# Optimization experiments

Measured on AMD Instinct MI355X. Metric: run time of the kernel, lower is better.

Reference implementation:

```python
import jax, jax.numpy as jnp
import numpy as np

SIGMA = 1.0
BN_EPS = 1e-5
N_OP, N_MACH, N_JOB = 200000, 1000, 20000
E_OM, E_JO, N_PAIRS = 1000000, 200000, 500000
H, D0 = 64, 32


def _bn(x, g, b):
    # BatchNorm1d, training-mode batch statistics over the node/row dim
    m = x.mean(0)
    v = x.var(0)
    return g * (x - m) * jax.lax.rsqrt(v + BN_EPS) + b


def _encode(x, W):
    # MultiPeriodicEncoder: learned frequencies, concat(sin, cos) -> 2*16 = 32 dims
    h = (x @ W) / SIGMA
    return jnp.concatenate([jnp.sin(h), jnp.cos(h)], axis=-1)


def _gin(x_dst, agg, eps, W1, b1, g1, be1, W2, b2):
    # GINConv: MLP((1+eps)*x + sum-aggregated messages); MLP = Lin->BN->ReLU->Lin
    h = ((1.0 + eps) * x_dst + agg) @ W1 + b1
    h = jax.nn.relu(_bn(h, g1, be1))
    return h @ W2 + b2


def _forward(x_operation, x_machine, x_job,
             W_enc_op, W_enc_mach, W_enc_job,
             gin_W1_l0, gin_W1_l12, gin_b1, gin_g1, gin_be1, gin_W2, gin_b2, gin_eps,
             Ws1, bs1, gs1, bes1, Ws2, bs2, gs2, bes2, Ws3, bs3,
             e_om_src, e_om_dst, e_mo_src, e_mo_dst, e_jo_src, e_jo_dst,
             e_oj_src, e_oj_dst, vp_op, vp_mach, vp_job):
    x_op = _encode(x_operation, W_enc_op)    # [N_OP, 32]
    x_ma = _encode(x_machine, W_enc_mach)    # [N_MACH, 32]
    x_jb = _encode(x_job, W_enc_job)         # [N_JOB, 32]
    num_layers = gin_eps.shape[0]
    for l in range(num_layers):
        def p(e):
            W1 = gin_W1_l0[e] if l == 0 else gin_W1_l12[l - 1, e]
            return (gin_eps[l, e], W1, gin_b1[l, e], gin_g1[l, e],
                    gin_be1[l, e], gin_W2[l, e], gin_b2[l, e])
        # edge-type order: 0=op->mach, 1=mach->op, 2=job->op, 3=op->job
        agg_mach = jax.ops.segment_sum(x_op[e_om_src], e_om_dst, num_segments=N_MACH)
        agg_op_mo = jax.ops.segment_sum(x_ma[e_mo_src], e_mo_dst, num_segments=N_OP)
        agg_op_jo = jax.ops.segment_sum(x_jb[e_jo_src], e_jo_dst, num_segments=N_OP)
        agg_job = jax.ops.segment_sum(x_op[e_oj_src], e_oj_dst, num_segments=N_JOB)
        new_ma = _gin(x_ma, agg_mach, *p(0))
        new_op = _gin(x_op, agg_op_mo, *p(1)) + _gin(x_op, agg_op_jo, *p(2))  # hetero 'sum'
        new_jb = _gin(x_jb, agg_job, *p(3))
        if l > 0:  # residual add of previous layer output (= current input)
            new_op = new_op + x_op
            new_ma = new_ma + x_ma
            new_jb = new_jb + x_jb
        x_op, x_ma, x_jb = new_op, new_ma, new_jb
    # gather by valid_pairs, concat in node-type order [operation, machine, job]
    feat = jnp.concatenate([x_op[vp_op], x_ma[vp_mach], x_jb[vp_job]], axis=1)  # [P, 192]
    h = jax.nn.relu(_bn(feat @ Ws1 + bs1, gs1, bes1))
    h = jax.nn.relu(_bn(h @ Ws2 + bs2, gs2, bes2))
    return (h @ Ws3 + bs3)[:, 0]


def setup_inputs() -> dict:
    key = jax.random.key(0)
    ks = jax.random.split(key, 24)
    rn = lambda k, s: jax.random.normal(k, s, dtype=jnp.float32) * 0.1
    return {
        'x_operation': jax.random.normal(ks[0], (N_OP, 8), dtype=jnp.float32),
        'x_machine': jax.random.normal(ks[1], (N_MACH, 4), dtype=jnp.float32),
        'x_job': jax.random.normal(ks[2], (N_JOB, 4), dtype=jnp.float32),
        'W_enc_op': rn(ks[3], (8, 16)),
        'W_enc_mach': rn(ks[4], (4, 16)),
        'W_enc_job': rn(ks[5], (4, 16)),
        'gin_W1_l0': rn(ks[6], (4, D0, H)),
        'gin_W1_l12': rn(ks[7], (2, 4, H, H)),
        'gin_b1': jnp.zeros((3, 4, H), jnp.float32),
        'gin_g1': jnp.ones((3, 4, H), jnp.float32),
        'gin_be1': jnp.zeros((3, 4, H), jnp.float32),
        'gin_W2': rn(ks[8], (3, 4, H, H)),
        'gin_b2': jnp.zeros((3, 4, H), jnp.float32),
        'gin_eps': jnp.zeros((3, 4), jnp.float32),
        'Ws1': rn(ks[9], (3 * H, H)),
        'bs1': jnp.zeros((H,), jnp.float32),
        'gs1': jnp.ones((H,), jnp.float32),
        'bes1': jnp.zeros((H,), jnp.float32),
        'Ws2': rn(ks[10], (H, H // 2)),
        'bs2': jnp.zeros((H // 2,), jnp.float32),
        'gs2': jnp.ones((H // 2,), jnp.float32),
        'bes2': jnp.zeros((H // 2,), jnp.float32),
        'Ws3': rn(ks[11], (H // 2, 1)),
        'bs3': jnp.zeros((1,), jnp.float32),
        'e_om_src': jax.random.randint(ks[12], (E_OM,), 0, N_OP),
        'e_om_dst': jax.random.randint(ks[13], (E_OM,), 0, N_MACH),
        'e_mo_src': jax.random.randint(ks[14], (E_OM,), 0, N_MACH),
        'e_mo_dst': jax.random.randint(ks[15], (E_OM,), 0, N_OP),
        'e_jo_src': jax.random.randint(ks[16], (E_JO,), 0, N_JOB),
        'e_jo_dst': jax.random.randint(ks[17], (E_JO,), 0, N_OP),
        'e_oj_src': jax.random.randint(ks[18], (E_JO,), 0, N_OP),
        'e_oj_dst': jax.random.randint(ks[19], (E_JO,), 0, N_JOB),
        'vp_op': jax.random.randint(ks[20], (N_PAIRS,), 0, N_OP),
        'vp_mach': jax.random.randint(ks[21], (N_PAIRS,), 0, N_MACH),
        'vp_job': jax.random.randint(ks[22], (N_PAIRS,), 0, N_JOB),
    }


def reference(x_operation, x_machine, x_job,
              W_enc_op, W_enc_mach, W_enc_job,
              gin_W1_l0, gin_W1_l12, gin_b1, gin_g1, gin_be1, gin_W2, gin_b2, gin_eps,
              Ws1, bs1, gs1, bes1, Ws2, bs2, gs2, bes2, Ws3, bs3,
              e_om_src, e_om_dst, e_mo_src, e_mo_dst, e_jo_src, e_jo_dst,
              e_oj_src, e_oj_dst, vp_op, vp_mach, vp_job):
    return _forward(x_operation, x_machine, x_job,
                    W_enc_op, W_enc_mach, W_enc_job,
                    gin_W1_l0, gin_W1_l12, gin_b1, gin_g1, gin_be1, gin_W2, gin_b2, gin_eps,
                    Ws1, bs1, gs1, bes1, Ws2, bs2, gs2, bes2, Ws3, bs3,
                    e_om_src, e_om_dst, e_mo_src, e_mo_dst, e_jo_src, e_jo_dst,
                    e_oj_src, e_oj_dst, vp_op, vp_mach, vp_job)
```

## Files before the change

kernel.cpp:

```cpp
#include <hip/hip_runtime.h>
#include <math.h>

#define N_OP_   200000
#define N_MACH_ 1000
#define N_JOB_  20000
#define E_OM_   1000000
#define E_JO_   200000
#define N_PAIRS_ 500000

#define B_OM_ 0
#define B_MO_ 64000
#define B_JO_ 264000
#define B_OJ_ 464000
#define TOTC_ 484000
#define E_TOT_ 2400000

#define GH_   1172
#define G_OP_ 782
#define G_MA_ 4
#define G_JB_ 79

#define CDIV(a,b) (((a)+(b)-1)/(b))

typedef __attribute__((ext_vector_type(8))) short short8v;
typedef __attribute__((ext_vector_type(4))) float f32x4;

__device__ __forceinline__ unsigned short f2bf(float f){
  unsigned int u = __float_as_uint(f);
  return (unsigned short)((u + 0x7fffu + ((u>>16)&1u)) >> 16);
}
__device__ __forceinline__ float bf2f(unsigned short h){
  return __uint_as_float(((unsigned int)h)<<16);
}

template<int DIN>
__device__ __forceinline__ void encode_body(const float* __restrict__ x,
    const float* __restrict__ W, float* __restrict__ out, int N, float* sW, int bid){
  if (threadIdx.x < DIN*16) sW[threadIdx.x] = W[threadIdx.x];
  __syncthreads();
  int i = bid*256 + threadIdx.x;
  if (i >= N) return;
  float xv[DIN];
#pragma unroll
  for (int k=0;k<DIN;k++) xv[k] = x[i*DIN+k];
#pragma unroll
  for (int j=0;j<16;j++){
    float h = 0.f;
#pragma unroll
    for (int k=0;k<DIN;k++) h = fmaf(xv[k], sW[k*16+j], h);
    float s, c;
    sincosf(h, &s, &c);
    out[(size_t)i*64 + j]      = s;
    out[(size_t)i*64 + 16 + j] = c;
  }
}

__device__ __forceinline__ int edge_cidx(int e,
    const int* __restrict__ eom_d, const int* __restrict__ emo_d,
    const int* __restrict__ ejo_d, const int* __restrict__ eoj_d){
  if (e < E_OM_)            return B_OM_ + eom_d[e]*64 + (e & 63);
  else if (e < 2*E_OM_)     return B_MO_ + emo_d[e - E_OM_];
  else if (e < 2*E_OM_+E_JO_) return B_JO_ + ejo_d[e - 2*E_OM_];
  else                      return B_OJ_ + eoj_d[e - 2*E_OM_ - E_JO_];
}
__device__ __forceinline__ int edge_src(int e,
    const int* __restrict__ eom_s, const int* __restrict__ emo_s,
    const int* __restrict__ ejo_s, const int* __restrict__ eoj_s){
  if (e < E_OM_)            return eom_s[e];
  else if (e < 2*E_OM_)     return emo_s[e - E_OM_];
  else if (e < 2*E_OM_+E_JO_) return ejo_s[e - 2*E_OM_];
  else                      return eoj_s[e - 2*E_OM_ - E_JO_];
}

__global__ __launch_bounds__(256) void enc_hist_kernel(
    const float* __restrict__ xop, const float* __restrict__ Wop, float* __restrict__ Pop,
    const float* __restrict__ xma, const float* __restrict__ Wma, float* __restrict__ Pma,
    const float* __restrict__ xjb, const float* __restrict__ Wjb, float* __restrict__ Pjb,
    const int* __restrict__ eom_d, const int* __restrict__ emo_d,
    const int* __restrict__ ejo_d, const int* __restrict__ eoj_d,
    int* __restrict__ cnt)
{
  __shared__ float sW[128];
  int b = blockIdx.x;
  if (b < GH_){
    const int gsz = GH_*256;
    int i0 = b*256 + threadIdx.x;
    for (int base = i0; base < E_TOT_; base += 8*gsz){
      int c[8]; bool act[8];
#pragma unroll
      for (int j=0;j<8;j++){
        int e = base + j*gsz;
        act[j] = (e < E_TOT_);
        if (act[j]) c[j] = edge_cidx(e, eom_d, emo_d, ejo_d, eoj_d);
      }
#pragma unroll
      for (int j=0;j<8;j++) if (act[j]) atomicAdd(&cnt[c[j]], 1);
    }
  } else if (b < GH_ + G_OP_){
    encode_body<8>(xop, Wop, Pop, N_OP_, sW, b - GH_);
  } else if (b < GH_ + G_OP_ + G_MA_){
    encode_body<4>(xma, Wma, Pma, N_MACH_, sW, b - GH_ - G_OP_);
  } else {
    encode_body<4>(xjb, Wjb, Pjb, N_JOB_, sW, b - GH_ - G_OP_ - G_MA_);
  }
}

__global__ __launch_bounds__(256) void fill_all_kernel(
    const int* __restrict__ eom_s, const int* __restrict__ eom_d,
    const int* __restrict__ emo_s, const int* __restrict__ emo_d,
    const int* __restrict__ ejo_s, const int* __restrict__ ejo_d,
    const int* __restrict__ eoj_s, const int* __restrict__ eoj_d,
    int* __restrict__ cursor, int* __restrict__ elist){
  int gsz = gridDim.x*blockDim.x;
  int i0 = blockIdx.x*blockDim.x + threadIdx.x;
  for (int base = i0; base < E_TOT_; base += 8*gsz){
    int cidx[8], src[8]; bool act[8];
#pragma unroll
    for (int j=0;j<8;j++){
      int e = base + j*gsz;
      act[j] = (e < E_TOT_);
      if (act[j]){
        cidx[j] = edge_cidx(e, eom_d, emo_d, ejo_d, eoj_d);
        src[j]  = edge_src (e, eom_s, emo_s, ejo_s, eoj_s);
      }
    }
    int p[8];
#pragma unroll
    for (int j=0;j<8;j++) if (act[j]) p[j] = atomicAdd(&cursor[cidx[j]], 1);
#pragma unroll
    for (int j=0;j<8;j++) if (act[j]) elist[p[j]] = src[j];
  }
}

__global__ void scan_block_sums(const int* __restrict__ cnt, int N, int* __restrict__ partials){
  __shared__ int red[256];
  int base = blockIdx.x*2048;
  int s = 0;
#pragma unroll
  for (int j=0;j<8;j++){ int i = base + threadIdx.x + j*256; if (i<N) s += cnt[i]; }
  red[threadIdx.x] = s; __syncthreads();
  for (int st=128; st>0; st>>=1){ if (threadIdx.x<st) red[threadIdx.x]+=red[threadIdx.x+st]; __syncthreads(); }
  if (threadIdx.x==0) partials[blockIdx.x] = red[0];
}

__global__ void scan_partials(int* __restrict__ partials, int NB, int* __restrict__ offN){
  __shared__ int buf[256];
  int v = (threadIdx.x < NB) ? partials[threadIdx.x] : 0;
  buf[threadIdx.x] = v; __syncthreads();
  int acc = v;
  for (int st=1; st<256; st<<=1){
    int t = (threadIdx.x >= st) ? buf[threadIdx.x-st] : 0;
    __syncthreads();
    acc += t; buf[threadIdx.x] = acc;
    __syncthreads();
  }
  if (threadIdx.x < NB) partials[threadIdx.x] = acc - v;
  if (threadIdx.x == NB-1) offN[0] = acc;
}

__global__ void scan_write_offsets(const int* __restrict__ cnt, int N,
    const int* __restrict__ partials, int* __restrict__ off){
  __shared__ int buf[256];
  int base = blockIdx.x*2048;
  int v[8]; int s = 0;
#pragma unroll
  for (int j=0;j<8;j++){ int i = base + threadIdx.x*8 + j; v[j] = (i<N)?cnt[i]:0; s += v[j]; }
  buf[threadIdx.x] = s; __syncthreads();
  int acc = s;
  for (int st=1; st<256; st<<=1){
    int t = (threadIdx.x >= st) ? buf[threadIdx.x-st] : 0;
    __syncthreads();
    acc += t; buf[threadIdx.x] = acc;
    __syncthreads();
  }
  int ex = partials[blockIdx.x] + acc - s;
#pragma unroll
  for (int j=0;j<8;j++){ int i = base + threadIdx.x*8 + j; if (i<N) off[i] = ex; ex += v[j]; }
}

__global__ __launch_bounds__(256) void agg_block_kernel(const int* __restrict__ off,
    const int* __restrict__ srcs, const float* __restrict__ feat,
    float* __restrict__ outp, int Ndst, int D){
  __shared__ float red[4][64];
  int m = blockIdx.x;
  if (m >= Ndst) return;
  int g = threadIdx.x >> 6, lane = threadIdx.x & 63;
  int s = off[m*64], e = off[m*64 + 64];
  float acc = 0.f;
  for (int base = s + g*64; base < e; base += 256){
    int cnt = e - base; if (cnt > 64) cnt = 64;
    int r = (lane < cnt) ? srcs[base + lane] : 0;
    int i = 0;
    for (; i + 4 <= cnt; i += 4){
      int r0 = __shfl(r, i), r1 = __shfl(r, i+1), r2 = __shfl(r, i+2), r3 = __shfl(r, i+3);
      float v0 = feat[(size_t)r0*64 + lane];
      float v1 = feat[(size_t)r1*64 + lane];
      float v2 = feat[(size_t)r2*64 + lane];
      float v3 = feat[(size_t)r3*64 + lane];
      acc += (v0 + v1) + (v2 + v3);
    }
    for (; i < cnt; i++){
      int ri = __shfl(r, i);
      acc += feat[(size_t)ri*64 + lane];
    }
  }
  red[g][lane] = acc;
  __syncthreads();
  if (g==0 && lane<D)
    outp[(size_t)m*64+lane] = red[0][lane]+red[1][lane]+red[2][lane]+red[3][lane];
}

template<int K>
__global__ __launch_bounds__(256,3) void partA_fused_kernel(
    const int* __restrict__ off_all, const int* __restrict__ elist,
    const float* __restrict__ Xop, const float* __restrict__ Xma, const float* __restrict__ Xjb,
    float* hm, float* ho1, float* ho2, float* hj,
    const float* __restrict__ Wm, const float* __restrict__ Wa,
    const float* __restrict__ Wb, const float* __restrict__ Wj,
    const float* __restrict__ bm, const float* __restrict__ ba,
    const float* __restrict__ bb, const float* __restrict__ bj,
    float* __restrict__ lstats,
    const float* __restrict__ epsp, int ebase)
{
  constexpr int KP = K + 4;
  constexpr int NF4 = K/16;
  __shared__ float sW[K][64];
  __shared__ float sZ[64][KP];
  __shared__ float sred[16][64];
  const int tid = threadIdx.x;
  const int lc = tid & 15, lr = tid >> 4;
  const int Tm = (N_MACH_+63)>>6, To = (N_OP_+63)>>6;
  int t = blockIdx.x;
  int seg, tile;
  if (t < Tm){ seg=0; tile=t; }
  else if (t < Tm+To){ seg=1; tile=t-Tm; }
  else if (t < Tm+2*To){ seg=2; tile=t-Tm-To; }
  else { seg=3; tile=t-Tm-2*To; }
  float* z            = seg==0?hm:seg==1?ho1:seg==2?ho2:hj;
  const float* x      = seg==0?Xma:seg==3?Xjb:Xop;
  const float* feat   = seg==0?Xop:seg==1?Xma:seg==2?Xjb:Xop;
  const float* W      = seg==0?Wm:seg==1?Wa:seg==2?Wb:Wj;
  const float* b      = seg==0?bm:seg==1?ba:seg==2?bb:bj;
  const int N         = seg==0?N_MACH_:seg==3?N_JOB_:N_OP_;
  const int* offs     = off_all + (seg==0?B_OM_:seg==1?B_MO_:seg==2?B_JO_:B_OJ_);
  float* st           = lstats + seg*128;
  const float e1 = 1.0f + epsp[ebase + seg];
  for (int idx = tid*4; idx < K*64; idx += 1024){
    int k = idx >> 6, c = idx & 63;
    *(float4*)&sW[k][c] = *(const float4*)&W[(size_t)k*64 + c];
  }
  float4 bias4 = *(const float4*)&b[lc*4];
  const int rbase = tile << 6;
  {
    const int r = tid >> 2, q = tid & 3;
    const int cbase = q*(K/4);
    int row = rbase + r;
    float4 a4[NF4];
#pragma unroll
    for (int f=0; f<NF4; f++) a4[f] = make_float4(0.f,0.f,0.f,0.f);
    if (row < N){
      if (seg == 0){
        const float4* H4 = (const float4*)&z[(size_t)row*64 + cbase];
#pragma unroll
        for (int f=0; f<NF4; f++) a4[f] = H4[f];
      } else {
        int s = offs[row], e = offs[row+1];
        int i = s;
        for (; i+2<=e; i+=2){
          int s0 = elist[i], s1 = elist[i+1];
          const float4* F0 = (const float4*)&feat[(size_t)s0*64 + cbase];
          const float4* F1 = (const float4*)&feat[(size_t)s1*64 + cbase];
          float4 v0[NF4], v1[NF4];
#pragma unroll
          for (int f=0; f<NF4; f++){ v0[f]=F0[f]; v1[f]=F1[f]; }
#pragma unroll
          for (int f=0; f<NF4; f++){
            a4[f].x += v0[f].x + v1[f].x;
            a4[f].y += v0[f].y + v1[f].y;
            a4[f].z += v0[f].z + v1[f].z;
            a4[f].w += v0[f].w + v1[f].w;
          }
        }
        if (i < e){
          int s0 = elist[i];
          const float4* F0 = (const float4*)&feat[(size_t)s0*64 + cbase];
#pragma unroll
          for (int f=0; f<NF4; f++){
            float4 v = F0[f];
            a4[f].x += v.x; a4[f].y += v.y; a4[f].z += v.z; a4[f].w += v.w;
          }
        }
      }
      const float4* X4 = (const float4*)&x[(size_t)row*64 + cbase];
#pragma unroll
      for (int f=0; f<NF4; f++){
        float4 xv = X4[f];
        a4[f].x = fmaf(e1, xv.x, a4[f].x);
        a4[f].y = fmaf(e1, xv.y, a4[f].y);
        a4[f].z = fmaf(e1, xv.z, a4[f].z);
        a4[f].w = fmaf(e1, xv.w, a4[f].w);
      }
    }
#pragma unroll
    for (int f=0; f<NF4; f++) *(float4*)&sZ[r][cbase + f*4] = a4[f];
  }
  __syncthreads();
  float acc[4][4];
#pragma unroll
  for (int i=0;i<4;i++){ acc[i][0]=0.f; acc[i][1]=0.f; acc[i][2]=0.f; acc[i][3]=0.f; }
#pragma unroll 2
  for (int kb = 0; kb < K/4; kb++){
    float4 zf[4], wf[4];
#pragma unroll
    for (int i=0;i<4;i++) zf[i] = *(const float4*)&sZ[lr*4+i][kb*4];
#pragma unroll
    for (int kk=0;kk<4;kk++) wf[kk] = *(const float4*)&sW[kb*4+kk][lc*4];
#pragma unroll
    for (int i=0;i<4;i++){
      acc[i][0] = fmaf(zf[i].x, wf[0].x, acc[i][0]);
      acc[i][1] = fmaf(zf[i].x, wf[0].y, acc[i][1]);
      acc[i][2] = fmaf(zf[i].x, wf[0].z, acc[i][2]);
      acc[i][3] = fmaf(zf[i].x, wf[0].w, acc[i][3]);
      acc[i][0] = fmaf(zf[i].y, wf[1].x, acc[i][0]);
      acc[i][1] = fmaf(zf[i].y, wf[1].y, acc[i][1]);
      acc[i][2] = fmaf(zf[i].y, wf[1].z, acc[i][2]);
      acc[i][3] = fmaf(zf[i].y, wf[1].w, acc[i][3]);
      acc[i][0] = fmaf(zf[i].z, wf[2].x, acc[i][0]);
      acc[i][1] = fmaf(zf[i].z, wf[2].y, acc[i][1]);
      acc[i][2] = fmaf(zf[i].z, wf[2].z, acc[i][2]);
      acc[i][3] = fmaf(zf[i].z, wf[2].w, acc[i][3]);
      acc[i][0] = fmaf(zf[i].w, wf[3].x, acc[i][0]);
      acc[i][1] = fmaf(zf[i].w, wf[3].y, acc[i][1]);
      acc[i][2] = fmaf(zf[i].w, wf[3].z, acc[i][2]);
      acc[i][3] = fmaf(zf[i].w, wf[3].w, acc[i][3]);
    }
  }
  float4 psum = make_float4(0.f,0.f,0.f,0.f), psq = make_float4(0.f,0.f,0.f,0.f);
#pragma unroll
  for (int i=0;i<4;i++){
    int row = rbase + lr*4 + i;
    if (row < N){
      float4 o;
      o.x = acc[i][0] + bias4.x;
      o.y = acc[i][1] + bias4.y;
      o.z = acc[i][2] + bias4.z;
      o.w = acc[i][3] + bias4.w;
      *(float4*)&z[(size_t)row*64 + lc*4] = o;
      psum.x += o.x; psum.y += o.y; psum.z += o.z; psum.w += o.w;
      psq.x += o.x*o.x; psq.y += o.y*o.y; psq.z += o.z*o.z; psq.w += o.w*o.w;
    }
  }
  __syncthreads();
  *(float4*)&sred[lr][lc*4] = psum;
  __syncthreads();
  if (tid < 64){
    float s = 0.f;
#pragma unroll
    for (int j=0;j<16;j++) s += sred[j][tid];
    atomicAdd(&st[tid], s);
  }
  __syncthreads();
  *(float4*)&sred[lr][lc*4] = psq;
  __syncthreads();
  if (tid < 64){
    float s = 0.f;
#pragma unroll
    for (int j=0;j<16;j++) s += sred[j][tid];
    atomicAdd(&st[64+tid], s);
  }
}

template<bool RESID>
__global__ __launch_bounds__(256,3) void partB_batch_kernel(
    float* h0, const float* x0, const float* W20, const float* b20, const float* sc0, int N0,
    float* hA, const float* hBp, const float* x1, const float* W2a, const float* W2b,
    const float* b2a_, const float* b2b_, const float* scA, const float* scB, int N1,
    float* h3, const float* x3, const float* W23, const float* b23, const float* sc3, int N3)
{
  __shared__ unsigned short sA[64][72];
  __shared__ unsigned short sB[64][72];
  const int tid = threadIdx.x;
  const int lane = tid & 63, w = tid >> 6;
  const int lo = lane & 15, hi = lane >> 4;
  const int T0=(N0+63)>>6, T1=(N1+63)>>6;
  int t = blockIdx.x;
  int seg, tile;
  if (t < T0){ seg=0; tile=t; }
  else if (t < T0+T1){ seg=1; tile=t-T0; }
  else { seg=2; tile=t-T0-T1; }
  const int N = seg==0?N0:seg==1?N1:N3;
  float* hout = seg==0?h0:seg==1?hA:h3;
  const float* x = seg==0?x0:seg==1?x1:x3;
  const int rbase = tile << 6;
  const int nsrc = (seg==1) ? 2 : 1;
  f32x4 acc[4];
#pragma unroll
  for (int n=0;n<4;n++) acc[n] = (f32x4){0.f,0.f,0.f,0.f};
  for (int s=0; s<nsrc; s++){
    const float* hsrc = (seg==1) ? (s==0? (const float*)hA : hBp)
                                 : (seg==0? (const float*)h0 : (const float*)h3);
    const float* Wp   = (seg==1) ? (s==0? W2a : W2b) : (seg==0? W20 : W23);
    const float* scp  = (seg==1) ? (s==0? scA : scB) : (seg==0? sc0 : sc3);
    __syncthreads();
    for (int idx = tid; idx < 1024; idx += 256){
      int k = idx >> 4, c4 = (idx & 15)*4;
      float4 wv = *(const float4*)&Wp[(size_t)k*64 + c4];
      sB[c4+0][k] = f2bf(wv.x);
      sB[c4+1][k] = f2bf(wv.y);
      sB[c4+2][k] = f2bf(wv.z);
      sB[c4+3][k] = f2bf(wv.w);
    }
    for (int idx = tid; idx < 1024; idx += 256){
      int r = idx >> 4, c4 = (idx & 15)*4;
      int row = rbase + r;
      ushort4 zz = make_ushort4(0,0,0,0);
      if (row < N){
        float4 hv = *(const float4*)&hsrc[(size_t)row*64 + c4];
        float4 sc4 = *(const float4*)&scp[c4];
        float4 sh4 = *(const float4*)&scp[64 + c4];
        float a0 = fmaf(sc4.x, hv.x, sh4.x); a0 = a0>0.f?a0:0.f;
        float a1 = fmaf(sc4.y, hv.y, sh4.y); a1 = a1>0.f?a1:0.f;
        float a2 = fmaf(sc4.z, hv.z, sh4.z); a2 = a2>0.f?a2:0.f;
        float a3 = fmaf(sc4.w, hv.w, sh4.w); a3 = a3>0.f?a3:0.f;
        zz = make_ushort4(f2bf(a0), f2bf(a1), f2bf(a2), f2bf(a3));
      }
      *(ushort4*)&sA[r][c4] = zz;
    }
    __syncthreads();
    short8v af0 = *(const short8v*)&sA[w*16 + lo][hi*8];
    short8v af1 = *(const short8v*)&sA[w*16 + lo][32 + hi*8];
#pragma unroll
    for (int n=0;n<4;n++){
      short8v bf0 = *(const short8v*)&sB[n*16 + lo][hi*8];
      short8v bf1 = *(const short8v*)&sB[n*16 + lo][32 + hi*8];
      acc[n] = __builtin_amdgcn_mfma_f32_16x16x32_bf16(af0, bf0, acc[n], 0, 0, 0);
      acc[n] = __builtin_amdgcn_mfma_f32_16x16x32_bf16(af1, bf1, acc[n], 0, 0, 0);
    }
  }
#pragma unroll
  for (int n=0;n<4;n++){
    int col = n*16 + lo;
    float bv;
    if (seg==1) bv = b2a_[col] + b2b_[col];
    else if (seg==0) bv = b20[col];
    else bv = b23[col];
#pragma unroll
    for (int j=0;j<4;j++){
      int row = rbase + w*16 + hi*4 + j;
      if (row < N){
        float v = acc[n][j] + bv;
        if (RESID) v += x[(size_t)row*64 + col];
        hout[(size_t)row*64 + col] = v;
      }
    }
  }
}

__global__ __launch_bounds__(256,3) void fp1_gemm_kernel(
    const float* __restrict__ Xop, const float* __restrict__ Xma, const float* __restrict__ Xjb,
    const int* __restrict__ vpo, const int* __restrict__ vpm, const int* __restrict__ vpj,
    const float* __restrict__ Ws1, const float* __restrict__ bs1,
    unsigned short* __restrict__ h1bf,
    int P, float* __restrict__ gsum, float* __restrict__ gsq)
{
  __shared__ unsigned short sA[64][72];
  __shared__ unsigned short sB[64][72];
  __shared__ float sred[16][64];
  const int tid = threadIdx.x;
  const int lane = tid & 63, w = tid >> 6;
  const int lo = lane & 15, hi = lane >> 4;
  float ps[4] = {0.f,0.f,0.f,0.f};
  float pq[4] = {0.f,0.f,0.f,0.f};
  const int ntiles = (P + 63) >> 6;
  for (int t = blockIdx.x; t < ntiles; t += gridDim.x){
    const int rbase = t << 6;
    f32x4 acc[4];
#pragma unroll
    for (int n=0;n<4;n++) acc[n] = (f32x4){0.f,0.f,0.f,0.f};
    for (int s=0; s<3; s++){
      const int* vps = (s==0) ? vpo : (s==1) ? vpm : vpj;
      const float* Xs = (s==0) ? Xop : (s==1) ? Xma : Xjb;
      __syncthreads();
      for (int idx = tid; idx < 1024; idx += 256){
        int k = idx >> 4, c4 = (idx & 15)*4;
        float4 wv = *(const float4*)&Ws1[(size_t)(s*64 + k)*64 + c4];
        sB[c4+0][k] = f2bf(wv.x);
        sB[c4+1][k] = f2bf(wv.y);
        sB[c4+2][k] = f2bf(wv.z);
        sB[c4+3][k] = f2bf(wv.w);
      }
      for (int idx = tid; idx < 1024; idx += 256){
        int r = idx >> 4, c4 = (idx & 15)*4;
        int row = rbase + r;
        ushort4 zz = make_ushort4(0,0,0,0);
        if (row < P){
          int nd = vps[row];
          float4 z = *(const float4*)&Xs[(size_t)nd*64 + c4];
          zz = make_ushort4(f2bf(z.x), f2bf(z.y), f2bf(z.z), f2bf(z.w));
        }
        *(ushort4*)&sA[r][c4] = zz;
      }
      __syncthreads();
      short8v af0 = *(const short8v*)&sA[w*16 + lo][hi*8];
      short8v af1 = *(const short8v*)&sA[w*16 + lo][32 + hi*8];
#pragma unroll
      for (int n=0;n<4;n++){
        short8v bf0 = *(const short8v*)&sB[n*16 + lo][hi*8];
        short8v bf1 = *(const short8v*)&sB[n*16 + lo][32 + hi*8];
        acc[n] = __builtin_amdgcn_mfma_f32_16x16x32_bf16(af0, bf0, acc[n], 0, 0, 0);
        acc[n] = __builtin_amdgcn_mfma_f32_16x16x32_bf16(af1, bf1, acc[n], 0, 0, 0);
      }
    }
#pragma unroll
    for (int n=0;n<4;n++){
      int col = n*16 + lo;
      float bv = bs1[col];
#pragma unroll
      for (int j=0;j<4;j++){
        int row = rbase + w*16 + hi*4 + j;
        if (row < P){
          float v = acc[n][j] + bv;
          h1bf[(size_t)row*64 + col] = f2bf(v);
          ps[n] += v; pq[n] += v*v;
        }
      }
    }
  }
  __syncthreads();
#pragma unroll
  for (int n=0;n<4;n++) sred[w*4 + hi][n*16 + lo] = ps[n];
  __syncthreads();
  if (tid < 64){
    float s = 0.f;
#pragma unroll
    for (int j=0;j<16;j++) s += sred[j][tid];
    atomicAdd(&gsum[tid], s);
  }
  __syncthreads();
#pragma unroll
  for (int n=0;n<4;n++) sred[w*4 + hi][n*16 + lo] = pq[n];
  __syncthreads();
  if (tid < 64){
    float s = 0.f;
#pragma unroll
    for (int j=0;j<16;j++) s += sred[j][tid];
    atomicAdd(&gsq[tid], s);
  }
}

__global__ __launch_bounds__(256,3) void fp2_lite_kernel(
    const float* __restrict__ scsh1,
    const float* __restrict__ Ws2, const float* __restrict__ bs2,
    const unsigned short* __restrict__ h1bf,
    float* __restrict__ s2out, int P,
    float* __restrict__ gsum2, float* __restrict__ gsq2)
{
  __shared__ float sZ[64][68];
  __shared__ float sW2[64][32];
  __shared__ float sred[16][64];
  const int tid = threadIdx.x;
  const int lc = tid & 15, lr = tid >> 4;
  for (int idx = tid*4; idx < 2048; idx += 1024){
    int k = idx >> 5, c = idx & 31;
    *(float4*)&sW2[k][c] = *(const float4*)&Ws2[(size_t)k*32 + c];
  }
  const float b2a = bs2[lc*2], b2b = bs2[lc*2+1];
  const int rbase = blockIdx.x << 6;
  for (int idx = tid*4; idx < 4096; idx += 1024){
    int r = idx >> 6, c = idx & 63;
    int row = rbase + r;
    float4 a = make_float4(0.f,0.f,0.f,0.f);
    if (row < P){
      ushort4 u = *(const ushort4*)&h1bf[(size_t)row*64 + c];
      float4 sc4 = *(const float4*)&scsh1[c];
      float4 sh4 = *(const float4*)&scsh1[64 + c];
      a.x = fmaf(sc4.x, bf2f(u.x), sh4.x); a.x = a.x > 0.f ? a.x : 0.f;
      a.y = fmaf(sc4.y, bf2f(u.y), sh4.y); a.y = a.y > 0.f ? a.y : 0.f;
      a.z = fmaf(sc4.z, bf2f(u.z), sh4.z); a.z = a.z > 0.f ? a.z : 0.f;
      a.w = fmaf(sc4.w, bf2f(u.w), sh4.w); a.w = a.w > 0.f ? a.w : 0.f;
    }
    *(float4*)&sZ[r][c] = a;
  }
  __syncthreads();
  float a2[4][2];
#pragma unroll
  for (int i=0;i<4;i++){ a2[i][0]=0.f; a2[i][1]=0.f; }
#pragma unroll 2
  for (int kb=0; kb<16; kb++){
    float4 zf[4];
    float2 wf[4];
#pragma unroll
    for (int i=0;i<4;i++) zf[i] = *(const float4*)&sZ[lr*4+i][kb*4];
#pragma unroll
    for (int kk=0;kk<4;kk++) wf[kk] = *(const float2*)&sW2[kb*4+kk][lc*2];
#pragma unroll
    for (int i=0;i<4;i++){
      a2[i][0] = fmaf(zf[i].x, wf[0].x, a2[i][0]);
      a2[i][1] = fmaf(zf[i].x, wf[0].y, a2[i][1]);
      a2[i][0] = fmaf(zf[i].y, wf[1].x, a2[i][0]);
      a2[i][1] = fmaf(zf[i].y, wf[1].y, a2[i][1]);
      a2[i][0] = fmaf(zf[i].z, wf[2].x, a2[i][0]);
      a2[i][1] = fmaf(zf[i].z, wf[2].y, a2[i][1]);
      a2[i][0] = fmaf(zf[i].w, wf[3].x, a2[i][0]);
      a2[i][1] = fmaf(zf[i].w, wf[3].y, a2[i][1]);
    }
  }
  float psum0=0.f, psum1=0.f, psq0=0.f, psq1=0.f;
#pragma unroll
  for (int i=0;i<4;i++){
    int row = rbase + lr*4 + i;
    if (row < P){
      float v0 = a2[i][0] + b2a;
      float v1 = a2[i][1] + b2b;
      *(float2*)&s2out[(size_t)row*32 + lc*2] = make_float2(v0, v1);
      psum0 += v0; psum1 += v1;
      psq0 += v0*v0; psq1 += v1*v1;
    }
  }
  __syncthreads();
  sred[lr][lc*2] = psum0; sred[lr][lc*2+1] = psum1;
  __syncthreads();
  if (tid < 32){
    float s = 0.f;
#pragma unroll
    for (int j=0;j<16;j++) s += sred[j][tid];
    atomicAdd(&gsum2[tid], s);
  }
  __syncthreads();
  sred[lr][lc*2] = psq0; sred[lr][lc*2+1] = psq1;
  __syncthreads();
  if (tid < 32){
    float s = 0.f;
#pragma unroll
    for (int j=0;j<16;j++) s += sred[j][tid];
    atomicAdd(&gsq2[tid], s);
  }
}

__global__ void bn_fin4_kernel(const float* __restrict__ stats,
    const float* __restrict__ g1, const float* __restrict__ be1, int l,
    float* __restrict__ scsh){
  int t = threadIdx.x;
  if (t >= 256) return;
  int gi = t>>6, c = t&63;
  float N = (gi==0) ? 1000.f : (gi==3) ? 20000.f : 200000.f;
  float invN = 1.f/N;
  float s = stats[gi*128 + c];
  float q = stats[gi*128 + 64 + c];
  float m = s*invN;
  float var = q*invN - m*m;
  float inv = rsqrtf(var + 1e-5f);
  float gg = g1[((size_t)l*4+gi)*64 + c];
  float bb = be1[((size_t)l*4+gi)*64 + c];
  float sc = gg*inv;
  scsh[gi*128 + c]      = sc;
  scsh[gi*128 + 64 + c] = bb - m*sc;
}

__global__ void bn_fin_kernel(const float* __restrict__ ssum, const float* __restrict__ ssq,
    const float* __restrict__ g, const float* __restrict__ be, float invN, int C,
    float* __restrict__ scsh){
  int c = threadIdx.x;
  if (c >= C) return;
  float m = ssum[c]*invN;
  float var = ssq[c]*invN - m*m;
  float inv = rsqrtf(var + 1e-5f);
  float s = g[c]*inv;
  scsh[c] = s; scsh[64+c] = be[c] - m*s;
}

__global__ __launch_bounds__(256) void final_pass3_kernel(
    const float* __restrict__ s2, const float* __restrict__ Ws3, const float* __restrict__ bs3,
    const float* __restrict__ scsh2,
    float* __restrict__ outp, int P){
  __shared__ float w3[32], c2[32], h2[32];
  __shared__ float b3;
  if (threadIdx.x < 32){
    w3[threadIdx.x]=Ws3[threadIdx.x];
    c2[threadIdx.x]=scsh2[threadIdx.x];
    h2[threadIdx.x]=scsh2[64+threadIdx.x];
  }
  if (threadIdx.x == 0) b3 = bs3[0];
  __syncthreads();
  int r = blockIdx.x*blockDim.x + threadIdx.x;
  if (r >= P) return;
  float acc = b3;
  const float4* S4 = (const float4*)(s2 + (size_t)r*32);
#pragma unroll
  for (int k4=0;k4<8;k4++){
    float4 v = S4[k4];
    float a;
    a = c2[4*k4+0]*v.x + h2[4*k4+0]; acc += (a>0.f?a:0.f)*w3[4*k4+0];
    a = c2[4*k4+1]*v.y + h2[4*k4+1]; acc += (a>0.f?a:0.f)*w3[4*k4+1];
    a = c2[4*k4+2]*v.z + h2[4*k4+2]; acc += (a>0.f?a:0.f)*w3[4*k4+2];
    a = c2[4*k4+3]*v.w + h2[4*k4+3]; acc += (a>0.f?a:0.f)*w3[4*k4+3];
  }
  outp[r] = acc;
}

extern "C" void kernel_launch(void* const* d_in, const int* in_sizes, int n_in,
                              void* d_out, int out_size, void* d_ws, size_t ws_size,
                              hipStream_t stream){
  (void)in_sizes; (void)n_in; (void)out_size; (void)ws_size;
  const float* x_op   = (const float*)d_in[0];
  const float* x_ma   = (const float*)d_in[1];
  const float* x_jb   = (const float*)d_in[2];
  const float* Wenc_op= (const float*)d_in[3];
  const float* Wenc_ma= (const float*)d_in[4];
  const float* Wenc_jb= (const float*)d_in[5];
  const float* gW1_l0 = (const float*)d_in[6];
  const float* gW1_l12= (const float*)d_in[7];
  const float* gb1    = (const float*)d_in[8];
  const float* gg1    = (const float*)d_in[9];
  const float* gbe1   = (const float*)d_in[10];
  const float* gW2    = (const float*)d_in[11];
  const float* gb2    = (const float*)d_in[12];
  const float* geps   = (const float*)d_in[13];
  const float* Ws1    = (const float*)d_in[14];
  const float* bs1    = (const float*)d_in[15];
  const float* gs1    = (const float*)d_in[16];
  const float* bes1   = (const float*)d_in[17];
  const float* Ws2    = (const float*)d_in[18];
  const float* bs2    = (const float*)d_in[19];
  const float* gs2    = (const float*)d_in[20];
  const float* bes2   = (const float*)d_in[21];
  const float* Ws3    = (const float*)d_in[22];
  const float* bs3    = (const float*)d_in[23];
  const int* eom_s = (const int*)d_in[24];
  const int* eom_d = (const int*)d_in[25];
  const int* emo_s = (const int*)d_in[26];
  const int* emo_d = (const int*)d_in[27];
  const int* ejo_s = (const int*)d_in[28];
  const int* ejo_d = (const int*)d_in[29];
  const int* eoj_s = (const int*)d_in[30];
  const int* eoj_d = (const int*)d_in[31];
  const int* vpo = (const int*)d_in[32];
  const int* vpm = (const int*)d_in[33];
  const int* vpj = (const int*)d_in[34];
  float* outp = (float*)d_out;

  char* wsp = (char*)d_ws;
  auto alloc = [&](size_t bytes)->void*{
    void* p = (void*)wsp;
    wsp += (bytes + 255) & ~(size_t)255;
    return p;
  };
  float* P0 = (float*)alloc((size_t)N_OP_*64*4);
  float* P1 = (float*)alloc((size_t)N_OP_*64*4);
  float* P2 = (float*)alloc((size_t)N_OP_*64*4);
  float* J0 = (float*)alloc((size_t)N_JOB_*64*4);
  float* J1 = (float*)alloc((size_t)N_JOB_*64*4);
  float* M0 = (float*)alloc((size_t)N_MACH_*64*4);
  float* M1 = (float*)alloc((size_t)N_MACH_*64*4);
  float* S2 = (float*)alloc((size_t)N_PAIRS_*32*4);
  int* off_all  = (int*)alloc((size_t)(TOTC_+1)*4);
  int* cnt_all  = (int*)alloc((size_t)TOTC_*4);
  int* elist_all= (int*)alloc((size_t)E_TOT_*4);
  int* partials = (int*)alloc(1024*4);
  float* lstats = (float*)alloc(512*4);
  float* lscsh  = (float*)alloc(512*4);
  float* fstats = (float*)alloc(512*4);

  hipMemsetAsync(cnt_all, 0, (size_t)TOTC_*4, stream);
  const int GTOT = GH_ + G_OP_ + G_MA_ + G_JB_;
  enc_hist_kernel<<<GTOT,256,0,stream>>>(
      x_op, Wenc_op, P0, x_ma, Wenc_ma, M0, x_jb, Wenc_jb, J0,
      eom_d, emo_d, ejo_d, eoj_d, cnt_all);
  const int NB = CDIV(TOTC_, 2048);
  scan_block_sums<<<NB,256,0,stream>>>(cnt_all, TOTC_, partials);
  scan_partials<<<1,256,0,stream>>>(partials, NB, off_all + TOTC_);
  scan_write_offsets<<<NB,256,0,stream>>>(cnt_all, TOTC_, partials, off_all);
  hipMemcpyAsync(cnt_all, off_all, (size_t)TOTC_*4, hipMemcpyDeviceToDevice, stream);
  fill_all_kernel<<<GH_,256,0,stream>>>(eom_s, eom_d, emo_s, emo_d,
                                        ejo_s, ejo_d, eoj_s, eoj_d,
                                        cnt_all, elist_all);

  float *Xop=P0, *Aop=P1, *Bop=P2;
  float *Xjb=J0, *Ajb=J1;
  float *Xma=M0, *Ama=M1;

  const int TA = CDIV(N_MACH_,64) + 2*CDIV(N_OP_,64) + CDIV(N_JOB_,64);
  const int TB = CDIV(N_MACH_,64) + CDIV(N_OP_,64) + CDIV(N_JOB_,64);

  for (int l=0; l<3; l++){
    int Din = (l==0) ? 32 : 64;
    hipMemsetAsync(lstats, 0, 512*4, stream);
    const float *W1m, *W1a, *W1b, *W1j;
    if (l==0){
      W1m = gW1_l0 + (size_t)0*32*64; W1a = gW1_l0 + (size_t)1*32*64;
      W1b = gW1_l0 + (size_t)2*32*64; W1j = gW1_l0 + (size_t)3*32*64;
    } else {
      W1m = gW1_l12 + ((size_t)(l-1)*4+0)*64*64; W1a = gW1_l12 + ((size_t)(l-1)*4+1)*64*64;
      W1b = gW1_l12 + ((size_t)(l-1)*4+2)*64*64; W1j = gW1_l12 + ((size_t)(l-1)*4+3)*64*64;
    }
    const float* b1m = gb1 + ((size_t)l*4+0)*64; const float* b1a = gb1 + ((size_t)l*4+1)*64;
    const float* b1b = gb1 + ((size_t)l*4+2)*64; const float* b1j = gb1 + ((size_t)l*4+3)*64;
    agg_block_kernel<<<N_MACH_,256,0,stream>>>(off_all + B_OM_, elist_all, Xop, Ama, N_MACH_, Din);
    if (l==0){
      partA_fused_kernel<32><<<TA,256,0,stream>>>(
        off_all, elist_all, Xop, Xma, Xjb,
        Ama, Aop, Bop, Ajb,
        W1m, W1a, W1b, W1j, b1m, b1a, b1b, b1j,
        lstats, geps, 0);
    } else {
      partA_fused_kernel<64><<<TA,256,0,stream>>>(
        off_all, elist_all, Xop, Xma, Xjb,
        Ama, Aop, Bop, Ajb,
        W1m, W1a, W1b, W1j, b1m, b1a, b1b, b1j,
        lstats, geps, l*4);
    }
    bn_fin4_kernel<<<1,256,0,stream>>>(lstats, gg1, gbe1, l, lscsh);
    const float* W2m = gW2 + ((size_t)l*4+0)*64*64; const float* b2m = gb2 + ((size_t)l*4+0)*64;
    const float* W2a = gW2 + ((size_t)l*4+1)*64*64; const float* b2a = gb2 + ((size_t)l*4+1)*64;
    const float* W2b = gW2 + ((size_t)l*4+2)*64*64; const float* b2b = gb2 + ((size_t)l*4+2)*64;
    const float* W2j = gW2 + ((size_t)l*4+3)*64*64; const float* b2j = gb2 + ((size_t)l*4+3)*64;
    if (l==0){
      partB_batch_kernel<false><<<TB,256,0,stream>>>(
        Ama, Xma, W2m, b2m, lscsh+0,   N_MACH_,
        Aop, Bop, Xop, W2a, W2b, b2a, b2b, lscsh+128, lscsh+256, N_OP_,
        Ajb, Xjb, W2j, b2j, lscsh+384, N_JOB_);
    } else {
      partB_batch_kernel<true><<<TB,256,0,stream>>>(
        Ama, Xma, W2m, b2m, lscsh+0,   N_MACH_,
        Aop, Bop, Xop, W2a, W2b, b2a, b2b, lscsh+128, lscsh+256, N_OP_,
        Ajb, Xjb, W2j, b2j, lscsh+384, N_JOB_);
    }
    { float* t=Xma; Xma=Ama; Ama=t; }
    { float* t=Xop; Xop=Aop; Aop=t; }
    { float* t=Xjb; Xjb=Ajb; Ajb=t; }
  }

  float* fsum1 = fstats;       float* fsq1 = fstats+64;
  float* fsum2 = fstats+128;   float* fsq2 = fstats+192;
  float* scsh1 = fstats+256;
  float* scsh2 = fstats+384;
  unsigned short* H1BF = (unsigned short*)S2;
  hipMemsetAsync(fstats, 0, 256*4, stream);
  fp1_gemm_kernel<<<2048,256,0,stream>>>(Xop,Xma,Xjb,vpo,vpm,vpj,Ws1,bs1,H1BF,N_PAIRS_,fsum1,fsq1);
  bn_fin_kernel<<<1,64,0,stream>>>(fsum1,fsq1,gs1,bes1, 1.f/(float)N_PAIRS_, 64, scsh1);
  fp2_lite_kernel<<<CDIV(N_PAIRS_,64),256,0,stream>>>(scsh1, Ws2, bs2, H1BF, S2, N_PAIRS_, fsum2, fsq2);
  bn_fin_kernel<<<1,32,0,stream>>>(fsum2,fsq2,gs2,bes2, 1.f/(float)N_PAIRS_, 32, scsh2);
  final_pass3_kernel<<<CDIV(N_PAIRS_,256),256,0,stream>>>(S2, Ws3, bs3, scsh2, outp, N_PAIRS_);
}
```

Baseline: 1.318 ms.

## Merge both op-node GIN edge types into one block and fuse offset copy

The fused part-A kernel now handles the two operation-destination edge types (mach->op and job->op) in a single block per 64-row tile. The operation-node input features are loaded once and reused for both aggregations and GEMMs, which halves the op-tile grid and avoids a duplicate read of Xop. The scan kernel also writes the cursor array directly, removing a device-to-device memcpy. In exchange each op block does twice the serial work with extra barriers, so there is less parallelism to hide gather latency.

```diff
diff --git a/kernel.cpp b/kernel.cpp
--- a/kernel.cpp
+++ b/kernel.cpp
@@ -159,7 +159,7 @@
 }
 
 __global__ void scan_write_offsets(const int* __restrict__ cnt, int N,
-    const int* __restrict__ partials, int* __restrict__ off){
+    const int* __restrict__ partials, int* __restrict__ off, int* __restrict__ cur){
   __shared__ int buf[256];
   int base = blockIdx.x*2048;
   int v[8]; int s = 0;
@@ -175,7 +175,11 @@
   }
   int ex = partials[blockIdx.x] + acc - s;
 #pragma unroll
-  for (int j=0;j<8;j++){ int i = base + threadIdx.x*8 + j; if (i<N) off[i] = ex; ex += v[j]; }
+  for (int j=0;j<8;j++){
+    int i = base + threadIdx.x*8 + j;
+    if (i<N){ off[i] = ex; cur[i] = ex; }
+    ex += v[j];
+  }
 }
 
 __global__ __launch_bounds__(256) void agg_block_kernel(const int* __restrict__ off,
@@ -211,110 +215,18 @@
 }
 
 template<int K>
-__global__ __launch_bounds__(256,3) void partA_fused_kernel(
-    const int* __restrict__ off_all, const int* __restrict__ elist,
-    const float* __restrict__ Xop, const float* __restrict__ Xma, const float* __restrict__ Xjb,
-    float* hm, float* ho1, float* ho2, float* hj,
-    const float* __restrict__ Wm, const float* __restrict__ Wa,
-    const float* __restrict__ Wb, const float* __restrict__ Wj,
-    const float* __restrict__ bm, const float* __restrict__ ba,
-    const float* __restrict__ bb, const float* __restrict__ bj,
-    float* __restrict__ lstats,
-    const float* __restrict__ epsp, int ebase)
-{
+__device__ __forceinline__ void tile_gemm(const float* sW, const float* sZ,
+    int lr, int lc, float acc[4][4]){
   constexpr int KP = K + 4;
-  constexpr int NF4 = K/16;
-  __shared__ float sW[K][64];
-  __shared__ float sZ[64][KP];
-  __shared__ float sred[16][64];
-  const int tid = threadIdx.x;
-  const int lc = tid & 15, lr = tid >> 4;
-  const int Tm = (N_MACH_+63)>>6, To = (N_OP_+63)>>6;
-  int t = blockIdx.x;
-  int seg, tile;
-  if (t < Tm){ seg=0; tile=t; }
-  else if (t < Tm+To){ seg=1; tile=t-Tm; }
-  else if (t < Tm+2*To){ seg=2; tile=t-Tm-To; }
-  else { seg=3; tile=t-Tm-2*To; }
-  float* z            = seg==0?hm:seg==1?ho1:seg==2?ho2:hj;
-  const float* x      = seg==0?Xma:seg==3?Xjb:Xop;
-  const float* feat   = seg==0?Xop:seg==1?Xma:seg==2?Xjb:Xop;
-  const float* W      = seg==0?Wm:seg==1?Wa:seg==2?Wb:Wj;
-  const float* b      = seg==0?bm:seg==1?ba:seg==2?bb:bj;
-  const int N         = seg==0?N_MACH_:seg==3?N_JOB_:N_OP_;
-  const int* offs     = off_all + (seg==0?B_OM_:seg==1?B_MO_:seg==2?B_JO_:B_OJ_);
-  float* st           = lstats + seg*128;
-  const float e1 = 1.0f + epsp[ebase + seg];
-  for (int idx = tid*4; idx < K*64; idx += 1024){
-    int k = idx >> 6, c = idx & 63;
-    *(float4*)&sW[k][c] = *(const float4*)&W[(size_t)k*64 + c];
-  }
-  float4 bias4 = *(const float4*)&b[lc*4];
-  const int rbase = tile << 6;
-  {
-    const int r = tid >> 2, q = tid & 3;
-    const int cbase = q*(K/4);
-    int row = rbase + r;
-    float4 a4[NF4];
-#pragma unroll
-    for (int f=0; f<NF4; f++) a4[f] = make_float4(0.f,0.f,0.f,0.f);
-    if (row < N){
-      if (seg == 0){
-        const float4* H4 = (const float4*)&z[(size_t)row*64 + cbase];
-#pragma unroll
-        for (int f=0; f<NF4; f++) a4[f] = H4[f];
-      } else {
-        int s = offs[row], e = offs[row+1];
-        int i = s;
-        for (; i+2<=e; i+=2){
-          int s0 = elist[i], s1 = elist[i+1];
-          const float4* F0 = (const float4*)&feat[(size_t)s0*64 + cbase];
-          const float4* F1 = (const float4*)&feat[(size_t)s1*64 + cbase];
-          float4 v0[NF4], v1[NF4];
-#pragma unroll
-          for (int f=0; f<NF4; f++){ v0[f]=F0[f]; v1[f]=F1[f]; }
-#pragma unroll
-          for (int f=0; f<NF4; f++){
-            a4[f].x += v0[f].x + v1[f].x;
-            a4[f].y += v0[f].y + v1[f].y;
-            a4[f].z += v0[f].z + v1[f].z;
-            a4[f].w += v0[f].w + v1[f].w;
-          }
-        }
-        if (i < e){
-          int s0 = elist[i];
-          const float4* F0 = (const float4*)&feat[(size_t)s0*64 + cbase];
-#pragma unroll
-          for (int f=0; f<NF4; f++){
-            float4 v = F0[f];
-            a4[f].x += v.x; a4[f].y += v.y; a4[f].z += v.z; a4[f].w += v.w;
-          }
-        }
-      }
-      const float4* X4 = (const float4*)&x[(size_t)row*64 + cbase];
-#pragma unroll
-      for (int f=0; f<NF4; f++){
-        float4 xv = X4[f];
-        a4[f].x = fmaf(e1, xv.x, a4[f].x);
-        a4[f].y = fmaf(e1, xv.y, a4[f].y);
-        a4[f].z = fmaf(e1, xv.z, a4[f].z);
-        a4[f].w = fmaf(e1, xv.w, a4[f].w);
-      }
-    }
-#pragma unroll
-    for (int f=0; f<NF4; f++) *(float4*)&sZ[r][cbase + f*4] = a4[f];
-  }
-  __syncthreads();
-  float acc[4][4];
 #pragma unroll
   for (int i=0;i<4;i++){ acc[i][0]=0.f; acc[i][1]=0.f; acc[i][2]=0.f; acc[i][3]=0.f; }
 #pragma unroll 2
   for (int kb = 0; kb < K/4; kb++){
     float4 zf[4], wf[4];
 #pragma unroll
-    for (int i=0;i<4;i++) zf[i] = *(const float4*)&sZ[lr*4+i][kb*4];
-#pragma unroll
-    for (int kk=0;kk<4;kk++) wf[kk] = *(const float4*)&sW[kb*4+kk][lc*4];
+    for (int i=0;i<4;i++) zf[i] = *(const float4*)&sZ[(lr*4+i)*KP + kb*4];
+#pragma unroll
+    for (int kk=0;kk<4;kk++) wf[kk] = *(const float4*)&sW[(kb*4+kk)*64 + lc*4];
 #pragma unroll
     for (int i=0;i<4;i++){
       acc[i][0] = fmaf(zf[i].x, wf[0].x, acc[i][0]);
@@ -335,6 +247,12 @@
       acc[i][3] = fmaf(zf[i].w, wf[3].w, acc[i][3]);
     }
   }
+}
+
+__device__ __forceinline__ void tile_epilogue_stats(float* z, const float* bias,
+    float (*sred)[64], float* st, int rbase, int N, int lr, int lc, int tid,
+    float acc[4][4]){
+  float4 bias4 = *(const float4*)&bias[lc*4];
   float4 psum = make_float4(0.f,0.f,0.f,0.f), psq = make_float4(0.f,0.f,0.f,0.f);
 #pragma unroll
   for (int i=0;i<4;i++){
@@ -367,6 +285,212 @@
 #pragma unroll
     for (int j=0;j<16;j++) s += sred[j][tid];
     atomicAdd(&st[64+tid], s);
+  }
+}
+
+template<int K>
+__global__ __launch_bounds__(256,3) void partA_fused_kernel(
+    const int* __restrict__ off_all, const int* __restrict__ elist,
+    const float* __restrict__ Xop, const float* __restrict__ Xma, const float* __restrict__ Xjb,
+    float* hm, float* hoA, float* hoB, float* hj,
+    const float* __restrict__ Wm, const float* __restrict__ Wa,
+    const float* __restrict__ Wb, const float* __restrict__ Wj,
+    const float* __restrict__ bm, const float* __restrict__ ba,
+    const float* __restrict__ bb, const float* __restrict__ bj,
+    float* __restrict__ lstats,
+    const float* __restrict__ epsp, int ebase)
+{
+  constexpr int KP = K + 4;
+  constexpr int NF4 = K/16;
+  __shared__ float sW[K*64];
+  __shared__ float sZ[64*KP];
+  __shared__ float sred[16][64];
+  const int tid = threadIdx.x;
+  const int lc = tid & 15, lr = tid >> 4;
+  const int Tm = (N_MACH_+63)>>6, To = (N_OP_+63)>>6;
+  int t = blockIdx.x;
+  const int r = tid >> 2, q = tid & 3;
+  const int cbase = q*(K/4);
+
+  if (t < Tm || t >= Tm + To){
+    const bool mach = (t < Tm);
+    const int tile = mach ? t : (t - Tm - To);
+    float* z           = mach ? hm : hj;
+    const float* x     = mach ? Xma : Xjb;
+    const float* feat  = Xop;
+    const float* W     = mach ? Wm : Wj;
+    const float* b     = mach ? bm : bj;
+    const int N        = mach ? N_MACH_ : N_JOB_;
+    const int* offs    = off_all + (mach ? B_OM_ : B_OJ_);
+    float* st          = lstats + (mach ? 0 : 3*128);
+    const float e1 = 1.0f + epsp[ebase + (mach ? 0 : 3)];
+    for (int idx = tid*4; idx < K*64; idx += 1024){
+      *(float4*)&sW[idx] = *(const float4*)&W[(size_t)(idx>>6)*64 + (idx&63)];
+    }
+    const int rbase = tile << 6;
+    {
+      int row = rbase + r;
+      float4 a4[NF4];
+#pragma unroll
+      for (int f=0; f<NF4; f++) a4[f] = make_float4(0.f,0.f,0.f,0.f);
+      if (row < N){
+        if (mach){
+          const float4* H4 = (const float4*)&z[(size_t)row*64 + cbase];
+#pragma unroll
+          for (int f=0; f<NF4; f++) a4[f] = H4[f];
+        } else {
+          int s = offs[row], e = offs[row+1];
+          int i = s;
+          for (; i+2<=e; i+=2){
+            int s0 = elist[i], s1 = elist[i+1];
+            const float4* F0 = (const float4*)&feat[(size_t)s0*64 + cbase];
+            const float4* F1 = (const float4*)&feat[(size_t)s1*64 + cbase];
+#pragma unroll
+            for (int f=0; f<NF4; f++){
+              float4 v0=F0[f], v1=F1[f];
+              a4[f].x += v0.x + v1.x; a4[f].y += v0.y + v1.y;
+              a4[f].z += v0.z + v1.z; a4[f].w += v0.w + v1.w;
+            }
+          }
+          if (i < e){
+            int s0 = elist[i];
+            const float4* F0 = (const float4*)&feat[(size_t)s0*64 + cbase];
+#pragma unroll
+            for (int f=0; f<NF4; f++){
+              float4 v = F0[f];
+              a4[f].x += v.x; a4[f].y += v.y; a4[f].z += v.z; a4[f].w += v.w;
+            }
+          }
+        }
+        const float4* X4 = (const float4*)&x[(size_t)row*64 + cbase];
+#pragma unroll
+        for (int f=0; f<NF4; f++){
+          float4 xv = X4[f];
+          a4[f].x = fmaf(e1, xv.x, a4[f].x);
+          a4[f].y = fmaf(e1, xv.y, a4[f].y);
+          a4[f].z = fmaf(e1, xv.z, a4[f].z);
+          a4[f].w = fmaf(e1, xv.w, a4[f].w);
+        }
+      }
+#pragma unroll
+      for (int f=0; f<NF4; f++) *(float4*)&sZ[r*KP + cbase + f*4] = a4[f];
+    }
+    __syncthreads();
+    float acc[4][4];
+    tile_gemm<K>(sW, sZ, lr, lc, acc);
+    tile_epilogue_stats(z, b, sred, st, rbase, N, lr, lc, tid, acc);
+  } else {
+    const int tile = t - Tm;
+    const int rbase = tile << 6;
+    const int row = rbase + r;
+    const float eA = 1.0f + epsp[ebase + 1];
+    const float eB = 1.0f + epsp[ebase + 2];
+    float4 xv4[NF4];
+#pragma unroll
+    for (int f=0; f<NF4; f++) xv4[f] = make_float4(0.f,0.f,0.f,0.f);
+    if (row < N_OP_){
+      const float4* X4 = (const float4*)&Xop[(size_t)row*64 + cbase];
+#pragma unroll
+      for (int f=0; f<NF4; f++) xv4[f] = X4[f];
+    }
+    for (int idx = tid*4; idx < K*64; idx += 1024){
+      *(float4*)&sW[idx] = *(const float4*)&Wa[(size_t)(idx>>6)*64 + (idx&63)];
+    }
+    {
+      float4 a4[NF4];
+#pragma unroll
+      for (int f=0; f<NF4; f++) a4[f] = make_float4(0.f,0.f,0.f,0.f);
+      if (row < N_OP_){
+        const int* offs = off_all + B_MO_;
+        int s = offs[row], e = offs[row+1];
+        int i = s;
+        for (; i+2<=e; i+=2){
+          int s0 = elist[i], s1 = elist[i+1];
+          const float4* F0 = (const float4*)&Xma[(size_t)s0*64 + cbase];
+          const float4* F1 = (const float4*)&Xma[(size_t)s1*64 + cbase];
+#pragma unroll
+          for (int f=0; f<NF4; f++){
+            float4 v0=F0[f], v1=F1[f];
+            a4[f].x += v0.x + v1.x; a4[f].y += v0.y + v1.y;
+            a4[f].z += v0.z + v1.z; a4[f].w += v0.w + v1.w;
+          }
+        }
+        if (i < e){
+          int s0 = elist[i];
+          const float4* F0 = (const float4*)&Xma[(size_t)s0*64 + cbase];
+#pragma unroll
+          for (int f=0; f<NF4; f++){
+            float4 v = F0[f];
+            a4[f].x += v.x; a4[f].y += v.y; a4[f].z += v.z; a4[f].w += v.w;
+          }
+        }
+#pragma unroll
+        for (int f=0; f<NF4; f++){
+          a4[f].x = fmaf(eA, xv4[f].x, a4[f].x);
+          a4[f].y = fmaf(eA, xv4[f].y, a4[f].y);
+          a4[f].z = fmaf(eA, xv4[f].z, a4[f].z);
+          a4[f].w = fmaf(eA, xv4[f].w, a4[f].w);
+        }
+      }
+#pragma unroll
+      for (int f=0; f<NF4; f++) *(float4*)&sZ[r*KP + cbase + f*4] = a4[f];
+    }
+    __syncthreads();
+    {
+      float acc[4][4];
+      tile_gemm<K>(sW, sZ, lr, lc, acc);
+      tile_epilogue_stats(hoA, ba, sred, lstats + 128, rbase, N_OP_, lr, lc, tid, acc);
+    }
+    __syncthreads();
+    for (int idx = tid*4; idx < K*64; idx += 1024){
+      *(float4*)&sW[idx] = *(const float4*)&Wb[(size_t)(idx>>6)*64 + (idx&63)];
+    }
+    {
+      float4 a4[NF4];
+#pragma unroll
+      for (int f=0; f<NF4; f++) a4[f] = make_float4(0.f,0.f,0.f,0.f);
+      if (row < N_OP_){
+        const int* offs = off_all + B_JO_;
+        int s = offs[row], e = offs[row+1];
+        int i = s;
+        for (; i+2<=e; i+=2){
+          int s0 = elist[i], s1 = elist[i+1];
+          const float4* F0 = (const float4*)&Xjb[(size_t)s0*64 + cbase];
+          const float4* F1 = (const float4*)&Xjb[(size_t)s1*64 + cbase];
+#pragma unroll
+          for (int f=0; f<NF4; f++){
+            float4 v0=F0[f], v1=F1[f];
+            a4[f].x += v0.x + v1.x; a4[f].y += v0.y + v1.y;
+            a4[f].z += v0.z + v1.z; a4[f].w += v0.w + v1.w;
+          }
+        }
+        if (i < e){
+          int s0 = elist[i];
+          const float4* F0 = (const float4*)&Xjb[(size_t)s0*64 + cbase];
+#pragma unroll
+          for (int f=0; f<NF4; f++){
+            float4 v = F0[f];
+            a4[f].x += v.x; a4[f].y += v.y; a4[f].z += v.z; a4[f].w += v.w;
+          }
+        }
+#pragma unroll
+        for (int f=0; f<NF4; f++){
+          a4[f].x = fmaf(eB, xv4[f].x, a4[f].x);
+          a4[f].y = fmaf(eB, xv4[f].y, a4[f].y);
+          a4[f].z = fmaf(eB, xv4[f].z, a4[f].z);
+          a4[f].w = fmaf(eB, xv4[f].w, a4[f].w);
+        }
+      }
+      __syncthreads();
+#pragma unroll
+      for (int f=0; f<NF4; f++) *(float4*)&sZ[r*KP + cbase + f*4] = a4[f];
+    }
+    __syncthreads();
+    {
+      float acc[4][4];
+      tile_gemm<K>(sW, sZ, lr, lc, acc);
+      tile_epilogue_stats(hoB, bb, sred, lstats + 256, rbase, N_OP_, lr, lc, tid, acc);
+    }
   }
 }
 
@@ -769,8 +893,7 @@
   const int NB = CDIV(TOTC_, 2048);
   scan_block_sums<<<NB,256,0,stream>>>(cnt_all, TOTC_, partials);
   scan_partials<<<1,256,0,stream>>>(partials, NB, off_all + TOTC_);
-  scan_write_offsets<<<NB,256,0,stream>>>(cnt_all, TOTC_, partials, off_all);
-  hipMemcpyAsync(cnt_all, off_all, (size_t)TOTC_*4, hipMemcpyDeviceToDevice, stream);
+  scan_write_offsets<<<NB,256,0,stream>>>(cnt_all, TOTC_, partials, off_all, cnt_all);
   fill_all_kernel<<<GH_,256,0,stream>>>(eom_s, eom_d, emo_s, emo_d,
                                         ejo_s, ejo_d, eoj_s, eoj_d,
                                         cnt_all, elist_all);
@@ -779,7 +902,7 @@
   float *Xjb=J0, *Ajb=J1;
   float *Xma=M0, *Ama=M1;
 
-  const int TA = CDIV(N_MACH_,64) + 2*CDIV(N_OP_,64) + CDIV(N_JOB_,64);
+  const int TA = CDIV(N_MACH_,64) + CDIV(N_OP_,64) + CDIV(N_JOB_,64);
   const int TB = CDIV(N_MACH_,64) + CDIV(N_OP_,64) + CDIV(N_JOB_,64);
 
   for (int l=0; l<3; l++){
```

After: 1.253 ms. -4.9%, faster.
